# Performance work log

Hardware: AMD Instinct MI355X
Metric: run time of the kernel (lower is better)

The kernel has to match this reference:

```python
import jax, jax.numpy as jnp
import numpy as np

LEAKY_SLOPE = 0.2

def gcn_conv(x, W, b, src, dst, deg_inv_sqrt, num_nodes):
    # GCNConv: out = D^{-1/2} (A+I) D^{-1/2} X W + b
    h = x @ W                                   # [N, out]
    norm = deg_inv_sqrt[src] * deg_inv_sqrt[dst]  # [E']
    msg = h[src] * norm[:, None]                # gather + scale
    out = jax.ops.segment_sum(msg, dst, num_segments=num_nodes)
    return out + b

def gcn_forward(x, edge_index, W1, b1, W2, b2, W3, b3):
    num_nodes = x.shape[0]
    loop = jnp.arange(num_nodes, dtype=edge_index.dtype)
    src = jnp.concatenate([edge_index[0], loop])  # add self-loops
    dst = jnp.concatenate([edge_index[1], loop])
    deg = jax.ops.segment_sum(jnp.ones_like(dst, dtype=x.dtype), dst,
                              num_segments=num_nodes)
    deg_inv_sqrt = jnp.where(deg > 0, jax.lax.rsqrt(deg), 0.0)
    # dropout is identity in eval mode (training=False)
    h = gcn_conv(x, W1, b1, src, dst, deg_inv_sqrt, num_nodes)
    h = jax.nn.leaky_relu(h, negative_slope=LEAKY_SLOPE)
    h = gcn_conv(h, W2, b2, src, dst, deg_inv_sqrt, num_nodes)
    h = jax.nn.leaky_relu(h, negative_slope=LEAKY_SLOPE)
    h = gcn_conv(h, W3, b3, src, dst, deg_inv_sqrt, num_nodes)
    return h

def setup_inputs() -> dict:
    key = jax.random.key(0)
    ks = jax.random.split(key, 8)
    N, F, E, C = 100000, 256, 3200000, 40
    x = jax.random.normal(ks[0], (N, F), dtype=jnp.float32)
    edge_index = jax.random.randint(ks[1], (2, E), 0, N, dtype=jnp.int64)
    W1 = jax.random.normal(ks[2], (F, 128), dtype=jnp.float32) * (1.0 / np.sqrt(F))
    b1 = jnp.zeros((128,), dtype=jnp.float32)
    W2 = jax.random.normal(ks[3], (128, 16), dtype=jnp.float32) * (1.0 / np.sqrt(128))
    b2 = jnp.zeros((16,), dtype=jnp.float32)
    W3 = jax.random.normal(ks[4], (16, C), dtype=jnp.float32) * (1.0 / np.sqrt(16))
    b3 = jnp.zeros((C,), dtype=jnp.float32)
    return {"x": x, "edge_index": edge_index, "W1": W1, "b1": b1,
            "W2": W2, "b2": b2, "W3": W3, "b3": b3}

def reference(x, edge_index, W1, b1, W2, b2, W3, b3):
    return gcn_forward(x, edge_index, W1, b1, W2, b2, W3, b3)
```

## Files before the change

### kernel.cpp

```cpp
#include <hip/hip_runtime.h>
#include <hip/hip_fp16.h>
#include <math.h>

#define LEAKY 0.2f
#define BP 6
#define BSZ 64
#define NBUK_MAX 2048

union H2 { __half2 h; int i; };
union H4 { __half2 h[2]; float2 f; };
union H8 { __half2 h[4]; float4 f; };

__device__ inline __half2 shfl_xor_h2(__half2 v, int m) {
    H2 u; u.h = v;
    u.i = __shfl_xor(u.i, m);
    return u.h;
}


__global__ __launch_bounds__(256) void khist(const int* __restrict__ dst,
                                             int* __restrict__ bhist,
                                             int E, int nbuk) {
    __shared__ int hist[NBUK_MAX];
    int t = threadIdx.x;
    for (int i = t; i < nbuk; i += 256) hist[i] = 0;
    __syncthreads();
    for (int e = blockIdx.x * 256 + t; e < E; e += gridDim.x * 256)
        atomicAdd(&hist[dst[e] >> BP], 1);
    __syncthreads();
    for (int i = t; i < nbuk; i += 256) {
        int v = hist[i];
        if (v) atomicAdd(&bhist[i], v);
    }
}

__global__ __launch_bounds__(1024) void bscan(const int* __restrict__ bhist,
                                              int* __restrict__ bbase,
                                              int* __restrict__ bcur, int nbuk) {
    __shared__ int s[1024];
    int t = threadIdx.x;
    int v[4]; int sum = 0;
    #pragma unroll
    for (int i = 0; i < 4; ++i) {
        int idx = t * 4 + i;
        v[i] = (idx < nbuk) ? bhist[idx] : 0;
        sum += v[i];
    }
    s[t] = sum; __syncthreads();
    for (int off = 1; off < 1024; off <<= 1) {
        int a = (t >= off) ? s[t - off] : 0;
        __syncthreads();
        s[t] += a;
        __syncthreads();
    }
    int run = (t > 0) ? s[t - 1] : 0;
    #pragma unroll
    for (int i = 0; i < 4; ++i) {
        int idx = t * 4 + i;
        if (idx < nbuk) { bbase[idx] = run; bcur[idx] = run; run += v[i]; }
    }
    if (t == 1023) bbase[nbuk] = s[1023];
}

__global__ __launch_bounds__(256) void kscatter2(const int* __restrict__ src,
                                                 const int* __restrict__ dst,
                                                 int* __restrict__ bcur,
                                                 int* __restrict__ ebuf,
                                                 int E, int nbuk, int chunk) {
    __shared__ int hist[NBUK_MAX];
    int t = threadIdx.x;
    int base = blockIdx.x * chunk;
    int end = min(base + chunk, E);
    for (int i = t; i < nbuk; i += 256) hist[i] = 0;
    __syncthreads();
    for (int e = base + t; e < end; e += 256)
        atomicAdd(&hist[dst[e] >> BP], 1);
    __syncthreads();
    for (int i = t; i < nbuk; i += 256) {
        int c = hist[i];
        hist[i] = c ? atomicAdd(&bcur[i], c) : 0;
    }
    __syncthreads();
    for (int e = base + t; e < end; e += 256) {
        int d = dst[e];
        int pos = atomicAdd(&hist[d >> BP], 1);
        ebuf[pos] = ((d & (BSZ - 1)) << 17) | src[e];
    }
}

__global__ __launch_bounds__(256) void kcount(const int* __restrict__ ebuf,
                                              const int* __restrict__ bbase,
                                              int* __restrict__ cnt,
                                              float* __restrict__ dis, int N) {
    __shared__ int h[BSZ];
    int b = blockIdx.x, t = threadIdx.x;
    if (t < BSZ) h[t] = 0;
    __syncthreads();
    int beg = bbase[b], end = bbase[b + 1];
    for (int j = beg + t; j < end; j += 256)
        atomicAdd(&h[(ebuf[j] >> 17) & (BSZ - 1)], 1);
    __syncthreads();
    if (t < BSZ) {
        int node = b * BSZ + t;
        if (node < N) {
            int c = h[t] + 1;
            cnt[node] = c;
            dis[node] = rsqrtf((float)c);
        }
    }
}

__global__ void scan_block(const int* __restrict__ cnt, int* rowptr, int* bsum, int n) {
    __shared__ int s[256];
    int t = threadIdx.x;
    int i = blockIdx.x * 256 + t;
    int v = (i < n) ? cnt[i] : 0;
    s[t] = v; __syncthreads();
    for (int off = 1; off < 256; off <<= 1) {
        int a = (t >= off) ? s[t - off] : 0;
        __syncthreads();
        s[t] += a;
        __syncthreads();
    }
    if (i < n) rowptr[i] = s[t] - v;
    if (t == 255) bsum[blockIdx.x] = s[255];
}

__global__ void scan_tops(int* bsum, int nb, int* rowptr, int n) {
    __shared__ int s[512];
    int t = threadIdx.x;
    int v = (t < nb) ? bsum[t] : 0;
    s[t] = v; __syncthreads();
    for (int off = 1; off < 512; off <<= 1) {
        int a = (t >= off) ? s[t - off] : 0;
        __syncthreads();
        s[t] += a;
        __syncthreads();
    }
    if (t < nb) bsum[t] = s[t] - v;
    if (t == 511) rowptr[n] = s[511];
}

__global__ void scan_add(int* rowptr, const int* __restrict__ bsum, int n) {
    int i = blockIdx.x * 256 + threadIdx.x;
    if (i < n) rowptr[i] += bsum[blockIdx.x];
}

__global__ __launch_bounds__(256) void kplace(const int* __restrict__ ebuf,
                                              const int* __restrict__ bbase,
                                              const int* __restrict__ rowptr,
                                              int* __restrict__ col, int N) {
    __shared__ int cur[BSZ];
    int b = blockIdx.x, t = threadIdx.x;
    if (t < BSZ) {
        int node = b * BSZ + t;
        if (node < N) {
            int r = rowptr[node];
            col[r] = node;
            cur[t] = r + 1;
        }
    }
    __syncthreads();
    int beg = bbase[b], end = bbase[b + 1];
    for (int j = beg + t; j < end; j += 256) {
        int v = ebuf[j];
        int dl = (v >> 17) & (BSZ - 1);
        int p = atomicAdd(&cur[dl], 1);
        col[p] = v & 0x1FFFF;
    }
}

__global__ __launch_bounds__(256) void gemm_256_128(
        const float* __restrict__ A, const float* __restrict__ B,
        const float* __restrict__ dis, __half* __restrict__ C, int M) {
    __shared__ __align__(16) __half As[16][72];
    __shared__ __align__(16) __half Bs[16][136];
    int t = threadIdx.x;
    int bm0 = blockIdx.x * 64;
    int lm  = t >> 2;
    int lk0 = (t & 3) * 4;
    int lbk  = t >> 4;
    int lbn0 = (t & 15) * 8;
    int arow = bm0 + lm;
    bool aval = arow < M;
    const float* Arow = A + (size_t)arow * 256;
    int tm0 = (t >> 5) * 8;
    int tn0 = (t & 31) * 4;
    __half2 acc[8][2];
    #pragma unroll
    for (int i = 0; i < 8; ++i) {
        acc[i][0] = __float2half2_rn(0.f);
        acc[i][1] = __float2half2_rn(0.f);
    }
    for (int kb = 0; kb < 256; kb += 16) {
        float4 av = make_float4(0.f, 0.f, 0.f, 0.f);
        if (aval) av = *(const float4*)(Arow + kb + lk0);
        float4 bv0 = *(const float4*)(B + (size_t)(kb + lbk) * 128 + lbn0);
        float4 bv1 = *(const float4*)(B + (size_t)(kb + lbk) * 128 + lbn0 + 4);
        As[lk0 + 0][lm] = __float2half(av.x);
        As[lk0 + 1][lm] = __float2half(av.y);
        As[lk0 + 2][lm] = __float2half(av.z);
        As[lk0 + 3][lm] = __float2half(av.w);
        H8 bu;
        bu.h[0] = __floats2half2_rn(bv0.x, bv0.y);
        bu.h[1] = __floats2half2_rn(bv0.z, bv0.w);
        bu.h[2] = __floats2half2_rn(bv1.x, bv1.y);
        bu.h[3] = __floats2half2_rn(bv1.z, bv1.w);
        *(float4*)&Bs[lbk][lbn0] = bu.f;
        __syncthreads();
        #pragma unroll
        for (int kk = 0; kk < 16; ++kk) {
            const __half2* ap = (const __half2*)&As[kk][tm0];
            __half2 a01 = ap[0], a23 = ap[1], a45 = ap[2], a67 = ap[3];
            const __half2* bp = (const __half2*)&Bs[kk][tn0];
            __half2 b01 = bp[0], b23 = bp[1];
            acc[0][0] = __hfma2(__low2half2(a01),  b01, acc[0][0]);
            acc[0][1] = __hfma2(__low2half2(a01),  b23, acc[0][1]);
            acc[1][0] = __hfma2(__high2half2(a01), b01, acc[1][0]);
            acc[1][1] = __hfma2(__high2half2(a01), b23, acc[1][1]);
            acc[2][0] = __hfma2(__low2half2(a23),  b01, acc[2][0]);
            acc[2][1] = __hfma2(__low2half2(a23),  b23, acc[2][1]);
            acc[3][0] = __hfma2(__high2half2(a23), b01, acc[3][0]);
            acc[3][1] = __hfma2(__high2half2(a23), b23, acc[3][1]);
            acc[4][0] = __hfma2(__low2half2(a45),  b01, acc[4][0]);
            acc[4][1] = __hfma2(__low2half2(a45),  b23, acc[4][1]);
            acc[5][0] = __hfma2(__high2half2(a45), b01, acc[5][0]);
            acc[5][1] = __hfma2(__high2half2(a45), b23, acc[5][1]);
            acc[6][0] = __hfma2(__low2half2(a67),  b01, acc[6][0]);
            acc[6][1] = __hfma2(__low2half2(a67),  b23, acc[6][1]);
            acc[7][0] = __hfma2(__high2half2(a67), b01, acc[7][0]);
            acc[7][1] = __hfma2(__high2half2(a67), b23, acc[7][1]);
        }
        __syncthreads();
    }
    #pragma unroll
    for (int i = 0; i < 8; ++i) {
        int r = bm0 + tm0 + i;
        if (r < M) {
            __half2 dh = __float2half2_rn(dis[r]);
            H4 o;
            o.h[0] = __hmul2(acc[i][0], dh);
            o.h[1] = __hmul2(acc[i][1], dh);
            *(float2*)(C + (size_t)r * 128 + tn0) = o.f;
        }
    }
}

__global__ __launch_bounds__(256) void prop128(
        const __half* __restrict__ h, const int* __restrict__ rowptr,
        const int* __restrict__ col, const float* __restrict__ dis,
        const float* __restrict__ bias, __half* __restrict__ out, int N) {
    int n = (blockIdx.x * 256 + threadIdx.x) >> 6;
    if (n >= N) return;
    int lane = threadIdx.x & 63;
    int eo = lane >> 4;
    int q = lane & 15;
    const float4* __restrict__ h4 = (const float4*)h;
    int beg = rowptr[n], end = rowptr[n + 1];
    __half2 acc[4];
    acc[0] = acc[1] = acc[2] = acc[3] = __float2half2_rn(0.f);
    int j = beg + eo;
    for (; j + 4 < end; j += 8) {
        int s0 = col[j];
        int s1 = col[j + 4];
        H8 u0, u1;
        u0.f = h4[(size_t)s0 * 16 + q];
        u1.f = h4[(size_t)s1 * 16 + q];
        acc[0] = __hadd2(acc[0], u0.h[0]);
        acc[1] = __hadd2(acc[1], u0.h[1]);
        acc[2] = __hadd2(acc[2], u0.h[2]);
        acc[3] = __hadd2(acc[3], u0.h[3]);
        acc[0] = __hadd2(acc[0], u1.h[0]);
        acc[1] = __hadd2(acc[1], u1.h[1]);
        acc[2] = __hadd2(acc[2], u1.h[2]);
        acc[3] = __hadd2(acc[3], u1.h[3]);
    }
    for (; j < end; j += 4) {
        int s = col[j];
        H8 u; u.f = h4[(size_t)s * 16 + q];
        acc[0] = __hadd2(acc[0], u.h[0]);
        acc[1] = __hadd2(acc[1], u.h[1]);
        acc[2] = __hadd2(acc[2], u.h[2]);
        acc[3] = __hadd2(acc[3], u.h[3]);
    }
    #pragma unroll
    for (int i = 0; i < 4; ++i) {
        acc[i] = __hadd2(acc[i], shfl_xor_h2(acc[i], 16));
        acc[i] = __hadd2(acc[i], shfl_xor_h2(acc[i], 32));
    }
    if (eo == 0) {
        float dn = dis[n];
        const float4* b4 = (const float4*)bias;
        float4 bA = b4[q * 2];
        float4 bB = b4[q * 2 + 1];
        float2 f0 = __half22float2(acc[0]);
        float2 f1 = __half22float2(acc[1]);
        float2 f2 = __half22float2(acc[2]);
        float2 f3 = __half22float2(acc[3]);
        float o0 = fmaf(dn, f0.x, bA.x), o1 = fmaf(dn, f0.y, bA.y);
        float o2 = fmaf(dn, f1.x, bA.z), o3 = fmaf(dn, f1.y, bA.w);
        float o4 = fmaf(dn, f2.x, bB.x), o5 = fmaf(dn, f2.y, bB.y);
        float o6 = fmaf(dn, f3.x, bB.z), o7 = fmaf(dn, f3.y, bB.w);
        o0 = o0 > 0.f ? o0 : LEAKY * o0;  o1 = o1 > 0.f ? o1 : LEAKY * o1;
        o2 = o2 > 0.f ? o2 : LEAKY * o2;  o3 = o3 > 0.f ? o3 : LEAKY * o3;
        o4 = o4 > 0.f ? o4 : LEAKY * o4;  o5 = o5 > 0.f ? o5 : LEAKY * o5;
        o6 = o6 > 0.f ? o6 : LEAKY * o6;  o7 = o7 > 0.f ? o7 : LEAKY * o7;
        H8 w;
        w.h[0] = __floats2half2_rn(o0, o1);
        w.h[1] = __floats2half2_rn(o2, o3);
        w.h[2] = __floats2half2_rn(o4, o5);
        w.h[3] = __floats2half2_rn(o6, o7);
        ((float4*)out)[(size_t)n * 16 + q] = w.f;
    }
}

__global__ __launch_bounds__(256) void gemm_128_16(
        const __half* __restrict__ A, const float* __restrict__ W,
        const float* __restrict__ dis, __half* __restrict__ C, int M) {
    __shared__ __align__(16) __half sxh[64 * 136];
    __shared__ float sw[128 * 16];
    int t = threadIdx.x;
    int n0 = blockIdx.x * 64;
    for (int i = t; i < 2048; i += 256) sw[i] = W[i];
    #pragma unroll
    for (int i = 0; i < 4; ++i) {
        int l = t + i * 256;
        int node = l >> 4, q = l & 15;
        int gn = n0 + node;
        float4 v = make_float4(0.f, 0.f, 0.f, 0.f);
        if (gn < M) v = ((const float4*)A)[(size_t)gn * 16 + q];
        *(float4*)&sxh[node * 136 + q * 8] = v;
    }
    __syncthreads();
    int n = t >> 2;
    int c0 = (t & 3) * 4;
    const float4* sw4 = (const float4*)sw;
    float4 acc = make_float4(0.f, 0.f, 0.f, 0.f);
    for (int k = 0; k < 128; k += 2) {
        __half2 xv2 = *(const __half2*)&sxh[n * 136 + k];
        float2 xf = __half22float2(xv2);
        float4 w0 = sw4[k * 4 + (t & 3)];
        float4 w1 = sw4[(k + 1) * 4 + (t & 3)];
        acc.x += xf.x * w0.x + xf.y * w1.x;
        acc.y += xf.x * w0.y + xf.y * w1.y;
        acc.z += xf.x * w0.z + xf.y * w1.z;
        acc.w += xf.x * w0.w + xf.y * w1.w;
    }
    int gn = n0 + n;
    if (gn < M) {
        float w = dis[gn];
        H4 o;
        o.h[0] = __floats2half2_rn(acc.x * w, acc.y * w);
        o.h[1] = __floats2half2_rn(acc.z * w, acc.w * w);
        *(float2*)(C + (size_t)gn * 16 + c0) = o.f;
    }
}

__global__ __launch_bounds__(256) void prop16(
        const __half* __restrict__ h, const int* __restrict__ rowptr,
        const int* __restrict__ col, const float* __restrict__ dis,
        const float* __restrict__ bias, void* __restrict__ outp,
        int N, int act, int post, int out_fp16) {
    int t = blockIdx.x * 256 + threadIdx.x;
    int n = t >> 4;
    if (n >= N) return;
    int li = threadIdx.x & 15;
    int eo = li >> 3;
    int hq = li & 7;
    const int* __restrict__ h2i = (const int*)h;
    int beg = rowptr[n], end = rowptr[n + 1];
    __half2 acc = __float2half2_rn(0.f);
    int j = beg + eo;
    for (; j + 6 < end; j += 8) {
        H2 u0, u1, u2, u3;
        u0.i = h2i[(size_t)col[j]     * 8 + hq];
        u1.i = h2i[(size_t)col[j + 2] * 8 + hq];
        u2.i = h2i[(size_t)col[j + 4] * 8 + hq];
        u3.i = h2i[(size_t)col[j + 6] * 8 + hq];
        acc = __hadd2(acc, u0.h);
        acc = __hadd2(acc, u1.h);
        acc = __hadd2(acc, u2.h);
        acc = __hadd2(acc, u3.h);
    }
    for (; j < end; j += 2) {
        H2 u; u.i = h2i[(size_t)col[j] * 8 + hq];
        acc = __hadd2(acc, u.h);
    }
    acc = __hadd2(acc, shfl_xor_h2(acc, 8));
    if (eo == 0) {
        float dn = dis[n];
        float2 f = __half22float2(acc);
        float ox = dn * f.x, oy = dn * f.y;
        if (act) {
            ox += bias[hq * 2];
            oy += bias[hq * 2 + 1];
            ox = ox > 0.f ? ox : LEAKY * ox;
            oy = oy > 0.f ? oy : LEAKY * oy;
        }
        if (post) { ox *= dn; oy *= dn; }
        if (out_fp16) {
            H2 w; w.h = __floats2half2_rn(ox, oy);
            ((int*)outp)[(size_t)n * 8 + hq] = w.i;
        } else {
            ((float2*)outp)[(size_t)n * 8 + hq] = make_float2(ox, oy);
        }
    }
}

__global__ __launch_bounds__(256) void gemm_16_40(
        const float* __restrict__ P, const float* __restrict__ W,
        const float* __restrict__ b, float* __restrict__ out, int total) {
    __shared__ float sw[16 * 40];
    __shared__ float sb[40];
    int t = threadIdx.x;
    for (int i = t; i < 640; i += 256) sw[i] = W[i];
    if (t < 40) sb[t] = b[t];
    __syncthreads();
    int idx = blockIdx.x * 256 + t;
    if (idx >= total) return;
    int n = idx / 40, c = idx % 40;
    float acc = sb[c];
    const float* pr = P + (size_t)n * 16;
    #pragma unroll
    for (int k = 0; k < 16; ++k) acc += pr[k] * sw[k * 40 + c];
    out[idx] = acc;
}


extern "C" void kernel_launch(void* const* d_in, const int* in_sizes, int n_in,
                              void* d_out, int out_size, void* d_ws, size_t ws_size,
                              hipStream_t stream) {
    const float* x  = (const float*)d_in[0];
    const int*   ei = (const int*)d_in[1];
    const float* W1 = (const float*)d_in[2];
    const float* b1 = (const float*)d_in[3];
    const float* W2 = (const float*)d_in[4];
    const float* b2 = (const float*)d_in[5];
    const float* W3 = (const float*)d_in[6];
    const float* b3 = (const float*)d_in[7];
    float* out = (float*)d_out;

    int N = in_sizes[0] / 256;
    int E = in_sizes[1] / 2;
    const int* src = ei;
    const int* dst = ei + E;
    int NBUK = (N + BSZ - 1) >> BP;

    char* w = (char*)d_ws;
    auto alloc = [&](size_t bytes) {
        char* p = w;
        w += (bytes + 255) & ~(size_t)255;
        return p;
    };
    int NB = (N + 255) / 256;
    int*    cnt     = (int*)   alloc((size_t)N * 4);
    int*    rowptr  = (int*)   alloc((size_t)(N + 1) * 4);
    int*    bsum    = (int*)   alloc((size_t)NB * 4);
    int*    bhist   = (int*)   alloc((size_t)NBUK * 4);
    int*    bbase   = (int*)   alloc((size_t)(NBUK + 1) * 4);
    int*    bcur    = (int*)   alloc((size_t)NBUK * 4);
    int*    ebuf    = (int*)   alloc((size_t)E * 4);
    int*    colx    = (int*)   alloc((size_t)(E + N) * 4);
    float*  dis     = (float*) alloc((size_t)N * 4);
    __half* h1h     = (__half*)alloc((size_t)N * 128 * 2);
    __half* x1h     = (__half*)alloc((size_t)N * 128 * 2);
    __half* h2h     = (__half*)alloc((size_t)N * 16 * 2);
    __half* x2h     = (__half*)alloc((size_t)N * 16 * 2);
    float*  p3      = (float*) alloc((size_t)N * 16 * 4);

    hipMemsetAsync(bhist, 0, (size_t)NBUK * 4, stream);
    khist   <<<256, 256, 0, stream>>>(dst, bhist, E, NBUK);
    bscan   <<<1, 1024, 0, stream>>>(bhist, bbase, bcur, NBUK);
    int SC_BLOCKS = 256;
    int chunk = (E + SC_BLOCKS - 1) / SC_BLOCKS;
    kscatter2<<<SC_BLOCKS, 256, 0, stream>>>(src, dst, bcur, ebuf, E, NBUK, chunk);
    kcount  <<<NBUK, 256, 0, stream>>>(ebuf, bbase, cnt, dis, N);
    scan_block<<<NB, 256, 0, stream>>>(cnt, rowptr, bsum, N);
    scan_tops <<<1, 512, 0, stream>>>(bsum, NB, rowptr, N);
    scan_add  <<<NB, 256, 0, stream>>>(rowptr, bsum, N);
    kplace  <<<NBUK, 256, 0, stream>>>(ebuf, bbase, rowptr, colx, N);

    gemm_256_128<<<(N + 63) / 64, 256, 0, stream>>>(x, W1, dis, h1h, N);
    prop128     <<<(N * 64 + 255) / 256, 256, 0, stream>>>(h1h, rowptr, colx,
                                                           dis, b1, x1h, N);
    gemm_128_16 <<<(N + 63) / 64, 256, 0, stream>>>(x1h, W2, dis, h2h, N);
    prop16      <<<(N * 16 + 255) / 256, 256, 0, stream>>>(h2h, rowptr, colx,
                                                           dis, b2, x2h, N, 1, 1, 1);
    prop16      <<<(N * 16 + 255) / 256, 256, 0, stream>>>(x2h, rowptr, colx,
                                                           dis, nullptr, p3, N, 0, 0, 0);
    gemm_16_40  <<<(N * 40 + 255) / 256, 256, 0, stream>>>(p3, W3, b3, out,
                                                           N * 40);
}
```

Before: 560.3 us.

## Replace packed-half GEMMs with MFMA kernels and unroll prop128 gather deeper

```diff
diff --git a/kernel.cpp b/kernel.cpp
--- a/kernel.cpp
+++ b/kernel.cpp
@@ -7,8 +7,10 @@
 #define BSZ 64
 #define NBUK_MAX 2048
 
+typedef _Float16 f16x8 __attribute__((ext_vector_type(8)));
+typedef float f32x4 __attribute__((ext_vector_type(4)));
+
 union H2 { __half2 h; int i; };
-union H4 { __half2 h[2]; float2 f; };
 union H8 { __half2 h[4]; float4 f; };
 
 __device__ inline __half2 shfl_xor_h2(__half2 v, int m) {
@@ -170,79 +172,98 @@
     }
 }
 
-__global__ __launch_bounds__(256) void gemm_256_128(
-        const float* __restrict__ A, const float* __restrict__ B,
+__global__ __launch_bounds__(256) void wtrans(const float* __restrict__ W1,
+                                              const float* __restrict__ W2,
+                                              __half* __restrict__ W1t,
+                                              __half* __restrict__ W2t) {
+    int idx = blockIdx.x * 256 + threadIdx.x;
+    if (idx < 32768) {
+        int n = idx >> 8, k = idx & 255;
+        W1t[idx] = __float2half(W1[k * 128 + n]);
+    } else if (idx < 32768 + 2048) {
+        int i = idx - 32768;
+        int n = i >> 7, k = i & 127;
+        W2t[i] = __float2half(W2[k * 16 + n]);
+    }
+}
+
+__global__ __launch_bounds__(256) void gemm1_mfma(
+        const float* __restrict__ x, const __half* __restrict__ W1t,
         const float* __restrict__ dis, __half* __restrict__ C, int M) {
-    __shared__ __align__(16) __half As[16][72];
-    __shared__ __align__(16) __half Bs[16][136];
-    int t = threadIdx.x;
-    int bm0 = blockIdx.x * 64;
-    int lm  = t >> 2;
-    int lk0 = (t & 3) * 4;
-    int lbk  = t >> 4;
-    int lbn0 = (t & 15) * 8;
-    int arow = bm0 + lm;
+    int wave = threadIdx.x >> 6;
+    int lane = threadIdx.x & 63;
+    int m = lane & 15, q = lane >> 4;
+    int row0 = (blockIdx.x * 4 + wave) * 16;
+    int arow = row0 + m;
     bool aval = arow < M;
-    const float* Arow = A + (size_t)arow * 256;
-    int tm0 = (t >> 5) * 8;
-    int tn0 = (t & 31) * 4;
-    __half2 acc[8][2];
-    #pragma unroll
-    for (int i = 0; i < 8; ++i) {
-        acc[i][0] = __float2half2_rn(0.f);
-        acc[i][1] = __float2half2_rn(0.f);
-    }
-    for (int kb = 0; kb < 256; kb += 16) {
-        float4 av = make_float4(0.f, 0.f, 0.f, 0.f);
-        if (aval) av = *(const float4*)(Arow + kb + lk0);
-        float4 bv0 = *(const float4*)(B + (size_t)(kb + lbk) * 128 + lbn0);
-        float4 bv1 = *(const float4*)(B + (size_t)(kb + lbk) * 128 + lbn0 + 4);
-        As[lk0 + 0][lm] = __float2half(av.x);
-        As[lk0 + 1][lm] = __float2half(av.y);
-        As[lk0 + 2][lm] = __float2half(av.z);
-        As[lk0 + 3][lm] = __float2half(av.w);
-        H8 bu;
-        bu.h[0] = __floats2half2_rn(bv0.x, bv0.y);
-        bu.h[1] = __floats2half2_rn(bv0.z, bv0.w);
-        bu.h[2] = __floats2half2_rn(bv1.x, bv1.y);
-        bu.h[3] = __floats2half2_rn(bv1.z, bv1.w);
-        *(float4*)&Bs[lbk][lbn0] = bu.f;
-        __syncthreads();
-        #pragma unroll
-        for (int kk = 0; kk < 16; ++kk) {
-            const __half2* ap = (const __half2*)&As[kk][tm0];
-            __half2 a01 = ap[0], a23 = ap[1], a45 = ap[2], a67 = ap[3];
-            const __half2* bp = (const __half2*)&Bs[kk][tn0];
-            __half2 b01 = bp[0], b23 = bp[1];
-            acc[0][0] = __hfma2(__low2half2(a01),  b01, acc[0][0]);
-            acc[0][1] = __hfma2(__low2half2(a01),  b23, acc[0][1]);
-            acc[1][0] = __hfma2(__high2half2(a01), b01, acc[1][0]);
-            acc[1][1] = __hfma2(__high2half2(a01), b23, acc[1][1]);
-            acc[2][0] = __hfma2(__low2half2(a23),  b01, acc[2][0]);
-            acc[2][1] = __hfma2(__low2half2(a23),  b23, acc[2][1]);
-            acc[3][0] = __hfma2(__high2half2(a23), b01, acc[3][0]);
-            acc[3][1] = __hfma2(__high2half2(a23), b23, acc[3][1]);
-            acc[4][0] = __hfma2(__low2half2(a45),  b01, acc[4][0]);
-            acc[4][1] = __hfma2(__low2half2(a45),  b23, acc[4][1]);
-            acc[5][0] = __hfma2(__high2half2(a45), b01, acc[5][0]);
-            acc[5][1] = __hfma2(__high2half2(a45), b23, acc[5][1]);
-            acc[6][0] = __hfma2(__low2half2(a67),  b01, acc[6][0]);
-            acc[6][1] = __hfma2(__low2half2(a67),  b23, acc[6][1]);
-            acc[7][0] = __hfma2(__high2half2(a67), b01, acc[7][0]);
-            acc[7][1] = __hfma2(__high2half2(a67), b23, acc[7][1]);
-        }
-        __syncthreads();
-    }
-    #pragma unroll
-    for (int i = 0; i < 8; ++i) {
-        int r = bm0 + tm0 + i;
-        if (r < M) {
-            __half2 dh = __float2half2_rn(dis[r]);
-            H4 o;
-            o.h[0] = __hmul2(acc[i][0], dh);
-            o.h[1] = __hmul2(acc[i][1], dh);
-            *(float2*)(C + (size_t)r * 128 + tn0) = o.f;
-        }
+    const float* xr = x + (size_t)arow * 256 + q * 8;
+    f32x4 acc[8];
+    #pragma unroll
+    for (int c = 0; c < 8; ++c) acc[c] = (f32x4){0.f, 0.f, 0.f, 0.f};
+    for (int k0 = 0; k0 < 256; k0 += 32) {
+        f16x8 a;
+        if (aval) {
+            float4 v0 = *(const float4*)(xr + k0);
+            float4 v1 = *(const float4*)(xr + k0 + 4);
+            a[0] = (_Float16)v0.x; a[1] = (_Float16)v0.y;
+            a[2] = (_Float16)v0.z; a[3] = (_Float16)v0.w;
+            a[4] = (_Float16)v1.x; a[5] = (_Float16)v1.y;
+            a[6] = (_Float16)v1.z; a[7] = (_Float16)v1.w;
+        } else {
+            #pragma unroll
+            for (int i = 0; i < 8; ++i) a[i] = (_Float16)0.f;
+        }
+        #pragma unroll
+        for (int c = 0; c < 8; ++c) {
+            f16x8 b = *(const f16x8*)(W1t + (size_t)(c * 16 + m) * 256 + k0 + q * 8);
+            acc[c] = __builtin_amdgcn_mfma_f32_16x16x32_f16(a, b, acc[c], 0, 0, 0);
+        }
+    }
+    float dw[4];
+    #pragma unroll
+    for (int r = 0; r < 4; ++r) {
+        int rr = row0 + q * 4 + r;
+        dw[r] = (rr < M) ? dis[rr] : 0.f;
+    }
+    #pragma unroll
+    for (int c = 0; c < 8; ++c) {
+        #pragma unroll
+        for (int r = 0; r < 4; ++r) {
+            int rr = row0 + q * 4 + r;
+            if (rr < M)
+                C[(size_t)rr * 128 + c * 16 + m] = __float2half(acc[c][r] * dw[r]);
+        }
+    }
+}
+
+__global__ __launch_bounds__(256) void gemm2_mfma(
+        const __half* __restrict__ A, const __half* __restrict__ W2t,
+        const float* __restrict__ dis, __half* __restrict__ C, int M) {
+    int wave = threadIdx.x >> 6;
+    int lane = threadIdx.x & 63;
+    int m = lane & 15, q = lane >> 4;
+    int row0 = (blockIdx.x * 4 + wave) * 16;
+    int arow = row0 + m;
+    bool aval = arow < M;
+    const __half* ar = A + (size_t)arow * 128 + q * 8;
+    f32x4 acc = (f32x4){0.f, 0.f, 0.f, 0.f};
+    #pragma unroll
+    for (int k0 = 0; k0 < 128; k0 += 32) {
+        f16x8 a;
+        if (aval) {
+            a = *(const f16x8*)(ar + k0);
+        } else {
+            #pragma unroll
+            for (int i = 0; i < 8; ++i) a[i] = (_Float16)0.f;
+        }
+        f16x8 b = *(const f16x8*)(W2t + (size_t)m * 128 + k0 + q * 8);
+        acc = __builtin_amdgcn_mfma_f32_16x16x32_f16(a, b, acc, 0, 0, 0);
+    }
+    #pragma unroll
+    for (int r = 0; r < 4; ++r) {
+        int rr = row0 + q * 4 + r;
+        if (rr < M)
+            C[(size_t)rr * 16 + m] = __float2half(acc[r] * dis[rr]);
     }
 }
 
@@ -260,28 +281,37 @@
     __half2 acc[4];
     acc[0] = acc[1] = acc[2] = acc[3] = __float2half2_rn(0.f);
     int j = beg + eo;
+    for (; j + 12 < end; j += 16) {
+        int s0 = col[j], s1 = col[j + 4], s2 = col[j + 8], s3 = col[j + 12];
+        H8 u0, u1, u2, u3;
+        u0.f = h4[(size_t)s0 * 16 + q];
+        u1.f = h4[(size_t)s1 * 16 + q];
+        u2.f = h4[(size_t)s2 * 16 + q];
+        u3.f = h4[(size_t)s3 * 16 + q];
+        #pragma unroll
+        for (int i = 0; i < 4; ++i) acc[i] = __hadd2(acc[i], u0.h[i]);
+        #pragma unroll
+        for (int i = 0; i < 4; ++i) acc[i] = __hadd2(acc[i], u1.h[i]);
+        #pragma unroll
+        for (int i = 0; i < 4; ++i) acc[i] = __hadd2(acc[i], u2.h[i]);
+        #pragma unroll
+        for (int i = 0; i < 4; ++i) acc[i] = __hadd2(acc[i], u3.h[i]);
+    }
     for (; j + 4 < end; j += 8) {
-        int s0 = col[j];
-        int s1 = col[j + 4];
+        int s0 = col[j], s1 = col[j + 4];
         H8 u0, u1;
         u0.f = h4[(size_t)s0 * 16 + q];
         u1.f = h4[(size_t)s1 * 16 + q];
-        acc[0] = __hadd2(acc[0], u0.h[0]);
-        acc[1] = __hadd2(acc[1], u0.h[1]);
-        acc[2] = __hadd2(acc[2], u0.h[2]);
-        acc[3] = __hadd2(acc[3], u0.h[3]);
-        acc[0] = __hadd2(acc[0], u1.h[0]);
-        acc[1] = __hadd2(acc[1], u1.h[1]);
-        acc[2] = __hadd2(acc[2], u1.h[2]);
-        acc[3] = __hadd2(acc[3], u1.h[3]);
+        #pragma unroll
+        for (int i = 0; i < 4; ++i) acc[i] = __hadd2(acc[i], u0.h[i]);
+        #pragma unroll
+        for (int i = 0; i < 4; ++i) acc[i] = __hadd2(acc[i], u1.h[i]);
     }
     for (; j < end; j += 4) {
         int s = col[j];
         H8 u; u.f = h4[(size_t)s * 16 + q];
-        acc[0] = __hadd2(acc[0], u.h[0]);
-        acc[1] = __hadd2(acc[1], u.h[1]);
-        acc[2] = __hadd2(acc[2], u.h[2]);
-        acc[3] = __hadd2(acc[3], u.h[3]);
+        #pragma unroll
+        for (int i = 0; i < 4; ++i) acc[i] = __hadd2(acc[i], u.h[i]);
     }
     #pragma unroll
     for (int i = 0; i < 4; ++i) {
@@ -311,48 +341,6 @@
         w.h[2] = __floats2half2_rn(o4, o5);
         w.h[3] = __floats2half2_rn(o6, o7);
         ((float4*)out)[(size_t)n * 16 + q] = w.f;
-    }
-}
-
-__global__ __launch_bounds__(256) void gemm_128_16(
-        const __half* __restrict__ A, const float* __restrict__ W,
-        const float* __restrict__ dis, __half* __restrict__ C, int M) {
-    __shared__ __align__(16) __half sxh[64 * 136];
-    __shared__ float sw[128 * 16];
-    int t = threadIdx.x;
-    int n0 = blockIdx.x * 64;
-    for (int i = t; i < 2048; i += 256) sw[i] = W[i];
-    #pragma unroll
-    for (int i = 0; i < 4; ++i) {
-        int l = t + i * 256;
-        int node = l >> 4, q = l & 15;
-        int gn = n0 + node;
-        float4 v = make_float4(0.f, 0.f, 0.f, 0.f);
-        if (gn < M) v = ((const float4*)A)[(size_t)gn * 16 + q];
-        *(float4*)&sxh[node * 136 + q * 8] = v;
-    }
-    __syncthreads();
-    int n = t >> 2;
-    int c0 = (t & 3) * 4;
-    const float4* sw4 = (const float4*)sw;
-    float4 acc = make_float4(0.f, 0.f, 0.f, 0.f);
-    for (int k = 0; k < 128; k += 2) {
-        __half2 xv2 = *(const __half2*)&sxh[n * 136 + k];
-        float2 xf = __half22float2(xv2);
-        float4 w0 = sw4[k * 4 + (t & 3)];
-        float4 w1 = sw4[(k + 1) * 4 + (t & 3)];
-        acc.x += xf.x * w0.x + xf.y * w1.x;
-        acc.y += xf.x * w0.y + xf.y * w1.y;
-        acc.z += xf.x * w0.z + xf.y * w1.z;
-        acc.w += xf.x * w0.w + xf.y * w1.w;
-    }
-    int gn = n0 + n;
-    if (gn < M) {
-        float w = dis[gn];
-        H4 o;
-        o.h[0] = __floats2half2_rn(acc.x * w, acc.y * w);
-        o.h[1] = __floats2half2_rn(acc.z * w, acc.w * w);
-        *(float2*)(C + (size_t)gn * 16 + c0) = o.f;
     }
 }
 
@@ -462,13 +450,16 @@
     int*    ebuf    = (int*)   alloc((size_t)E * 4);
     int*    colx    = (int*)   alloc((size_t)(E + N) * 4);
     float*  dis     = (float*) alloc((size_t)N * 4);
+    __half* W1t     = (__half*)alloc((size_t)128 * 256 * 2);
+    __half* W2t     = (__half*)alloc((size_t)16 * 128 * 2);
     __half* h1h     = (__half*)alloc((size_t)N * 128 * 2);
     __half* x1h     = (__half*)alloc((size_t)N * 128 * 2);
     __half* h2h     = (__half*)alloc((size_t)N * 16 * 2);
     __half* x2h     = (__half*)alloc((size_t)N * 16 * 2);
     float*  p3      = (float*) alloc((size_t)N * 16 * 4);
 
-    hipMemsetAsync(bhist, 0, (size_t)NBUK * 4, stream);
+    (void)hipMemsetAsync(bhist, 0, (size_t)NBUK * 4, stream);
+    wtrans  <<<136, 256, 0, stream>>>(W1, W2, W1t, W2t);
     khist   <<<256, 256, 0, stream>>>(dst, bhist, E, NBUK);
     bscan   <<<1, 1024, 0, stream>>>(bhist, bbase, bcur, NBUK);
     int SC_BLOCKS = 256;
@@ -480,14 +471,15 @@
     scan_add  <<<NB, 256, 0, stream>>>(rowptr, bsum, N);
     kplace  <<<NBUK, 256, 0, stream>>>(ebuf, bbase, rowptr, colx, N);
 
-    gemm_256_128<<<(N + 63) / 64, 256, 0, stream>>>(x, W1, dis, h1h, N);
-    prop128     <<<(N * 64 + 255) / 256, 256, 0, stream>>>(h1h, rowptr, colx,
-                                                           dis, b1, x1h, N);
-    gemm_128_16 <<<(N + 63) / 64, 256, 0, stream>>>(x1h, W2, dis, h2h, N);
-    prop16      <<<(N * 16 + 255) / 256, 256, 0, stream>>>(h2h, rowptr, colx,
-                                                           dis, b2, x2h, N, 1, 1, 1);
-    prop16      <<<(N * 16 + 255) / 256, 256, 0, stream>>>(x2h, rowptr, colx,
-                                                           dis, nullptr, p3, N, 0, 0, 0);
-    gemm_16_40  <<<(N * 40 + 255) / 256, 256, 0, stream>>>(p3, W3, b3, out,
-                                                           N * 40);
-}
+    int gtiles = (N + 63) / 64;
+    gemm1_mfma<<<gtiles, 256, 0, stream>>>(x, W1t, dis, h1h, N);
+    prop128   <<<(N * 64 + 255) / 256, 256, 0, stream>>>(h1h, rowptr, colx,
+                                                         dis, b1, x1h, N);
+    gemm2_mfma<<<gtiles, 256, 0, stream>>>(x1h, W2t, dis, h2h, N);
+    prop16    <<<(N * 16 + 255) / 256, 256, 0, stream>>>(h2h, rowptr, colx,
+                                                         dis, b2, x2h, N, 1, 1, 1);
+    prop16    <<<(N * 16 + 255) / 256, 256, 0, stream>>>(x2h, rowptr, colx,
+                                                         dis, nullptr, p3, N, 0, 0, 0);
+    gemm_16_40<<<(N * 40 + 255) / 256, 256, 0, stream>>>(p3, W3, b3, out,
+                                                         N * 40);
+}
```

Result: no change. 562.4 us (+0.4%).
